# Optimization experiments

Hardware: AMD Instinct MI355X
Metric: run time of the kernel (lower is better)

Reference implementation:

```python
import jax, jax.numpy as jnp
import numpy as np

WINDOW = 7
EPS = 1e-8


def setup_inputs() -> dict:
    key = jax.random.key(0)
    k1, k2, k3 = jax.random.split(key, 3)
    x = jax.random.normal(k1, (8, 256, 64, 64), dtype=jnp.float32)
    # 1x1 conv weights (bias=False): [out_ch, in_ch]
    w_reduce = jax.random.normal(k2, (64, 256), dtype=jnp.float32) * 0.05
    w_proj = jax.random.normal(k3, (512, 64), dtype=jnp.float32) * 0.1
    return {"x": x, "w_reduce": w_reduce, "w_proj": w_proj}


def _unfold_window(feat, window):
    # feat: [b, c, h, w] -> patches: [b, c, window*window, h, w]
    b, c, h, w = feat.shape
    pad = window // 2
    fp = jnp.pad(feat, ((0, 0), (0, 0), (pad, pad), (pad, pad)))
    # fixed small loop over window^2 = 49 shifts (matches F.unfold ordering)
    return jnp.stack(
        [fp[:, :, i:i + h, j:j + w] for i in range(window) for j in range(window)],
        axis=2,
    )


def reference(x, w_reduce, w_proj):
    window = WINDOW
    # reduce: 1x1 conv, no bias
    feat = jnp.einsum('oc,bchw->bohw', w_reduce, x)  # [b, cr, h, w]
    patches = _unfold_window(feat, window)           # [b, cr, K, h, w], K=49
    # cosine similarity between center feature and each window patch (dim=channel)
    dot = jnp.einsum('bchw,bckhw->bkhw', feat, patches)          # [b, K, h, w]
    cn = jnp.sqrt(jnp.sum(feat * feat, axis=1))                  # [b, h, w]
    pn = jnp.sqrt(jnp.sum(patches * patches, axis=1))            # [b, K, h, w]
    sim = dot / jnp.maximum(cn[:, None] * pn, EPS)               # [b, K, h, w]
    att = jax.nn.softmax(sim, axis=1)                            # softmax over window dim
    corr = jnp.einsum('bkhw,bckhw->bchw', att, patches)          # [b, cr, h, w]
    # proj: 1x1 conv, no bias
    return jnp.einsum('oc,bchw->bohw', w_proj, corr)             # [b, out, h, w]
```

## Files before the change

kernel.cpp:

```cpp
#include <hip/hip_runtime.h>
#include <stdint.h>

#define NPIX 4096
#define CIN  256
#define CR   64
#define COUT 512
#define NB   8
#define CG   256
#define FT   128

typedef _Float16 half8 __attribute__((ext_vector_type(8)));
typedef float f32x4 __attribute__((ext_vector_type(4)));

__device__ __forceinline__ float dpp8_sum(float d) {
  int y;
  y = __builtin_amdgcn_update_dpp(0, __float_as_int(d), 0xB1, 0xF, 0xF, true);
  d += __int_as_float(y);
  y = __builtin_amdgcn_update_dpp(0, __float_as_int(d), 0x4E, 0xF, 0xF, true);
  d += __int_as_float(y);
  y = __builtin_amdgcn_update_dpp(0, __float_as_int(d), 0x141, 0xF, 0xF, true);
  d += __int_as_float(y);
  return d;
}

__global__ __launch_bounds__(256) void k0_prep(
    const float* __restrict__ wr, const float* __restrict__ wp,
    _Float16* __restrict__ wrAh, _Float16* __restrict__ wrAl,
    _Float16* __restrict__ wpH,
    float* __restrict__ cnormG, float* __restrict__ featTail)
{
  const int tid = blockIdx.x * 256 + threadIdx.x;
  if (tid < 16384) {
    const int j = tid & 7, l = (tid >> 3) & 63;
    const int kt = (tid >> 9) & 7, mt = tid >> 12;
    const int m = mt * 16 + (l & 15);
    const int k = kt * 32 + (l >> 4) * 8 + j;
    const float v = wr[m * CIN + k];
    const _Float16 h = (_Float16)v;
    wrAh[tid] = h;
    wrAl[tid] = (_Float16)(v - (float)h);
  } else if (tid < 16384 + COUT * CR) {
    const int fi = tid - 16384;
    const int j = fi & 7, l = (fi >> 3) & 63;
    const int kt = (fi >> 9) & 1, ot = (fi >> 10) & 3, g = fi >> 12;
    const int o = g * 64 + ot * 16 + (l & 15);
    const int k = kt * 32 + (l >> 4) * 8 + j;
    wpH[fi] = (_Float16)wp[o * CR + k];
  } else {
    const int gi = tid - (16384 + COUT * CR);
    if (gi < CG)               cnormG[gi] = 0.f;
    else if (gi < 2 * CG)      cnormG[CG + NB * NPIX + (gi - CG)] = 0.f;
    else if (gi < 2 * CG + FT) featTail[gi - 2 * CG] = 0.f;
  }
}

__global__ __launch_bounds__(512) void k1_reduce(
    const float* __restrict__ x,
    const _Float16* __restrict__ wrAh, const _Float16* __restrict__ wrAl,
    float* __restrict__ feat, float* __restrict__ cnorm)
{
  const int blk = blockIdx.x;
  const int b = blk >> 6, seg = blk & 63;
  const int t = threadIdx.x, lane = t & 63;
  const int g = __builtin_amdgcn_readfirstlane((int)t >> 6);
  const int nt = g & 3, mth = g >> 2;
  const int col = lane & 15, krow = lane >> 4;

  const float* xb = x + (size_t)b * CIN * NPIX + seg * 64 + nt * 16 + col;

  f32x4 c0 = {0.f, 0.f, 0.f, 0.f};
  f32x4 c1 = {0.f, 0.f, 0.f, 0.f};

#pragma unroll
  for (int kt = 0; kt < 8; ++kt) {
    half8 Bh, Bl;
    const float* xk = xb + (size_t)(kt * 32 + krow * 8) * NPIX;
#pragma unroll
    for (int j = 0; j < 8; ++j) {
      const float v = xk[(size_t)j * NPIX];
      const _Float16 h = (_Float16)v;
      Bh[j] = h;
      Bl[j] = (_Float16)(v - (float)h);
    }
    const int fi0 = ((mth * 2 + 0) * 8 + kt) * 512 + lane * 8;
    const int fi1 = ((mth * 2 + 1) * 8 + kt) * 512 + lane * 8;
    const half8 Ah0 = *(const half8*)(wrAh + fi0);
    const half8 Al0 = *(const half8*)(wrAl + fi0);
    const half8 Ah1 = *(const half8*)(wrAh + fi1);
    const half8 Al1 = *(const half8*)(wrAl + fi1);
    c0 = __builtin_amdgcn_mfma_f32_16x16x32_f16(Ah0, Bh, c0, 0, 0, 0);
    c0 = __builtin_amdgcn_mfma_f32_16x16x32_f16(Ah0, Bl, c0, 0, 0, 0);
    c0 = __builtin_amdgcn_mfma_f32_16x16x32_f16(Al0, Bh, c0, 0, 0, 0);
    c1 = __builtin_amdgcn_mfma_f32_16x16x32_f16(Ah1, Bh, c1, 0, 0, 0);
    c1 = __builtin_amdgcn_mfma_f32_16x16x32_f16(Ah1, Bl, c1, 0, 0, 0);
    c1 = __builtin_amdgcn_mfma_f32_16x16x32_f16(Al1, Bh, c1, 0, 0, 0);
  }

  float p = 0.f;
  float* fbase = feat + (size_t)b * CR * NPIX + seg * 64 + nt * 16 + col;
#pragma unroll
  for (int r = 0; r < 4; ++r) {
    const int m0 = (mth * 2 + 0) * 16 + krow * 4 + r;
    const int m1 = (mth * 2 + 1) * 16 + krow * 4 + r;
    fbase[(size_t)m0 * NPIX] = c0[r];
    fbase[(size_t)m1 * NPIX] = c1[r];
    p = fmaf(c0[r], c0[r], p);
    p = fmaf(c1[r], c1[r], p);
  }
  p += __shfl_xor(p, 16);
  p += __shfl_xor(p, 32);

  __shared__ float cn[8][16];
  if (lane < 16) cn[g][lane] = p;
  __syncthreads();
  if (t < 64) {
    const int nt2 = t >> 4, c16 = t & 15;
    cnorm[b * NPIX + seg * 64 + t] = sqrtf(cn[nt2][c16] + cn[nt2 + 4][c16]);
  }
}

__global__ __launch_bounds__(512, 4) void k23_fused(
    const float* __restrict__ feat, const float* __restrict__ cnorm,
    const _Float16* __restrict__ wpH, float* __restrict__ out)
{
  const int blk = blockIdx.x;
  const int b = blk & 7, h = blk >> 3;
  const int t = threadIdx.x;
  const int lane = t & 63;
  const int g = __builtin_amdgcn_readfirstlane((int)t >> 6);
  const int w = t >> 3;
  const int cb = (t & 7) * 8;
  const int px = h * 64 + w;
  const int gpx = b * NPIX + px;

  const float* fb = feat + (size_t)b * CR * NPIX;
  const float* cnb = cnorm + b * NPIX;

  __shared__ float fs[2][72][68];
  __shared__ float cnS[2][80];
  __shared__ __align__(16) _Float16 corrH[4096];

  float rA[2][4];
  float rB[4];
  float rc = 0.f;
  const int jt = 64 + (t >> 4), c4t = t & 15;

  auto LOAD = [&](int ar) {
    const int base = ar * 64 - 4;
#pragma unroll
    for (int k = 0; k < 2; ++k) {
      const int c4 = g * 2 + k;
#pragma unroll
      for (int q = 0; q < 4; ++q)
        rA[k][q] = fb[(size_t)(c4 * 4 + q) * NPIX + base + lane];
    }
    if (t < 128) {
#pragma unroll
      for (int q = 0; q < 4; ++q)
        rB[q] = fb[(size_t)(c4t * 4 + q) * NPIX + base + jt];
    }
    if (t < 72) rc = cnb[base + t];
  };
  auto WRITE = [&](int bufi) {
#pragma unroll
    for (int k = 0; k < 2; ++k) {
      const int c4 = g * 2 + k;
      *(float4*)&fs[bufi][lane][c4 * 4] =
          make_float4(rA[k][0], rA[k][1], rA[k][2], rA[k][3]);
    }
    if (t < 128)
      *(float4*)&fs[bufi][jt][c4t * 4] = make_float4(rB[0], rB[1], rB[2], rB[3]);
    if (t < 72) cnS[bufi][t] = rc;
  };

  const float* fpx = fb + (size_t)cb * NPIX + px;
  float fc[8];
#pragma unroll
  for (int i = 0; i < 8; ++i) fc[i] = fpx[i * NPIX];
  const float cnc = cnorm[gpx];

  float acc[8];
#pragma unroll
  for (int i = 0; i < 8; ++i) acc[i] = 0.f;

  const int lo = (h - 3 < 0) ? 0 : h - 3;
  const int hi = (h + 3 > 63) ? 63 : h + 3;
  float l = 7.0f * (float)(6 - (hi - lo));

  LOAD(lo);
  WRITE(0);
  __syncthreads();

  int buf = 0;
  for (int ar = lo; ar <= hi; ++ar) {
    if (ar < hi) LOAD(ar + 1);
#pragma unroll
    for (int dx = -3; dx <= 3; ++dx) {
      const int j = w + 4 + dx;
      const float4 nv0 = *(const float4*)&fs[buf][j][cb];
      const float4 nv1 = *(const float4*)&fs[buf][j][cb + 4];
      float d = fmaf(fc[0], nv0.x,
                fmaf(fc[1], nv0.y,
                fmaf(fc[2], nv0.z,
                fmaf(fc[3], nv0.w,
                fmaf(fc[4], nv1.x,
                fmaf(fc[5], nv1.y,
                fmaf(fc[6], nv1.z, fc[7] * nv1.w)))))));
      d = dpp8_sum(d);
      const float cnk = cnS[buf][j];
      float sim = d * __builtin_amdgcn_rcpf(fmaxf(cnc * cnk, 1e-8f));
      const bool valid = (unsigned)(w + dx) < 64u;
      sim = valid ? sim : 0.f;
      const float p = __expf(sim);
      l += p;
      const float pv = valid ? p : 0.f;
      acc[0] = fmaf(pv, nv0.x, acc[0]);
      acc[1] = fmaf(pv, nv0.y, acc[1]);
      acc[2] = fmaf(pv, nv0.z, acc[2]);
      acc[3] = fmaf(pv, nv0.w, acc[3]);
      acc[4] = fmaf(pv, nv1.x, acc[4]);
      acc[5] = fmaf(pv, nv1.y, acc[5]);
      acc[6] = fmaf(pv, nv1.z, acc[6]);
      acc[7] = fmaf(pv, nv1.w, acc[7]);
    }
    if (ar < hi) WRITE(buf ^ 1);
    __syncthreads();
    buf ^= 1;
  }

  {
    const float inv = __builtin_amdgcn_rcpf(l);
    half8 hv;
#pragma unroll
    for (int i = 0; i < 8; ++i) hv[i] = (_Float16)(acc[i] * inv);
    const int wbyte = (w * 128 + (cb << 1)) ^ ((w & 7) << 4);
    *(half8*)((char*)corrH + wbyte) = hv;
  }
  __syncthreads();

  const _Float16* wA = wpH + (size_t)g * 4096;
  float* outb = out + ((size_t)b * COUT + g * 64) * NPIX + h * 64;
#pragma unroll
  for (int pt = 0; pt < 4; ++pt) {
    half8 Bf0, Bf1;
    {
      const int pxl = pt * 16 + (lane & 15);
      const int sw = (pxl & 7) << 4;
      const int rowb = pxl * 128 + ((lane >> 4) << 4);
      Bf0 = *(const half8*)((const char*)corrH + (rowb ^ sw));
      Bf1 = *(const half8*)((const char*)corrH + ((rowb + 64) ^ sw));
    }
#pragma unroll
    for (int ot = 0; ot < 4; ++ot) {
      f32x4 c = {0.f, 0.f, 0.f, 0.f};
      const half8 A0 = *(const half8*)(wA + (ot * 2 + 0) * 512 + lane * 8);
      const half8 A1 = *(const half8*)(wA + (ot * 2 + 1) * 512 + lane * 8);
      c = __builtin_amdgcn_mfma_f32_16x16x32_f16(A0, Bf0, c, 0, 0, 0);
      c = __builtin_amdgcn_mfma_f32_16x16x32_f16(A1, Bf1, c, 0, 0, 0);
      float* op = outb + (size_t)(ot * 16 + ((lane >> 4) << 2)) * NPIX
                       + pt * 16 + (lane & 15);
#pragma unroll
      for (int r = 0; r < 4; ++r) op[(size_t)r * NPIX] = c[r];
    }
  }
}

extern "C" void kernel_launch(void* const* d_in, const int* in_sizes, int n_in,
                              void* d_out, int out_size, void* d_ws, size_t ws_size,
                              hipStream_t stream)
{
  const float* x  = (const float*)d_in[0];
  const float* wr = (const float*)d_in[1];
  const float* wp = (const float*)d_in[2];
  float* out = (float*)d_out;

  float* ws = (float*)d_ws;
  _Float16* wrAh  = (_Float16*)ws;
  _Float16* wrAl  = (_Float16*)(ws + 8192);
  _Float16* wpH   = (_Float16*)(ws + 16384);
  float* cnormG   = ws + 32768;
  float* cnorm    = cnormG + CG;
  float* feat     = cnorm + NB * NPIX + CG;
  float* featTail = feat + (size_t)NB * CR * NPIX;

  hipLaunchKernelGGL(k0_prep,   dim3(195), dim3(256), 0, stream, wr, wp, wrAh, wrAl, wpH, cnormG, featTail);
  hipLaunchKernelGGL(k1_reduce, dim3(512), dim3(512), 0, stream, x, wrAh, wrAl, feat, cnorm);
  hipLaunchKernelGGL(k23_fused, dim3(512), dim3(512), 0, stream, feat, cnorm, wpH, out);
}
```

Measured before the change: 46.19 us.

## Store reduced features as fp16 pixel-major and use packed half math

The intermediate feature tensor is now stored as fp16 in a pixel-major [b][pixel][channel] layout instead of fp32 channel-major. This halves its global traffic and makes row loads into shared memory contiguous. The window loop uses fdot2 for the dot products and packed half2 FMAs for the weighted accumulation, split across two accumulator sets. The cost is lower precision in both the cosine similarities and the accumulated correlation sums, which may exceed the output tolerance. cnorm is still computed in fp32.

Result: faster. 41.10 us (-11.0%).

```diff
diff --git a/kernel.cpp b/kernel.cpp
--- a/kernel.cpp
+++ b/kernel.cpp
@@ -10,6 +10,8 @@
 #define FT   128
 
 typedef _Float16 half8 __attribute__((ext_vector_type(8)));
+typedef _Float16 half4 __attribute__((ext_vector_type(4)));
+typedef _Float16 half2v __attribute__((ext_vector_type(2)));
 typedef float f32x4 __attribute__((ext_vector_type(4)));
 
 __device__ __forceinline__ float dpp8_sum(float d) {
@@ -57,7 +59,7 @@
 __global__ __launch_bounds__(512) void k1_reduce(
     const float* __restrict__ x,
     const _Float16* __restrict__ wrAh, const _Float16* __restrict__ wrAl,
-    float* __restrict__ feat, float* __restrict__ cnorm)
+    _Float16* __restrict__ feat_h, float* __restrict__ cnorm)
 {
   const int blk = blockIdx.x;
   const int b = blk >> 6, seg = blk & 63;
@@ -96,17 +98,21 @@
     c1 = __builtin_amdgcn_mfma_f32_16x16x32_f16(Al1, Bh, c1, 0, 0, 0);
   }
 
+  const int px = seg * 64 + nt * 16 + col;
+  _Float16* fb = feat_h + ((size_t)b * NPIX + px) * 64;
+  const int ch0 = mth * 32 + krow * 4;
+  half4 v0, v1;
   float p = 0.f;
-  float* fbase = feat + (size_t)b * CR * NPIX + seg * 64 + nt * 16 + col;
 #pragma unroll
   for (int r = 0; r < 4; ++r) {
-    const int m0 = (mth * 2 + 0) * 16 + krow * 4 + r;
-    const int m1 = (mth * 2 + 1) * 16 + krow * 4 + r;
-    fbase[(size_t)m0 * NPIX] = c0[r];
-    fbase[(size_t)m1 * NPIX] = c1[r];
+    v0[r] = (_Float16)c0[r];
+    v1[r] = (_Float16)c1[r];
     p = fmaf(c0[r], c0[r], p);
     p = fmaf(c1[r], c1[r], p);
   }
+  *(half4*)(fb + ch0) = v0;
+  *(half4*)(fb + ch0 + 16) = v1;
+
   p += __shfl_xor(p, 16);
   p += __shfl_xor(p, 32);
 
@@ -120,7 +126,7 @@
 }
 
 __global__ __launch_bounds__(512, 4) void k23_fused(
-    const float* __restrict__ feat, const float* __restrict__ cnorm,
+    const _Float16* __restrict__ feat_h, const float* __restrict__ cnorm,
     const _Float16* __restrict__ wpH, float* __restrict__ out)
 {
   const int blk = blockIdx.x;
@@ -133,55 +139,41 @@
   const int px = h * 64 + w;
   const int gpx = b * NPIX + px;
 
-  const float* fb = feat + (size_t)b * CR * NPIX;
   const float* cnb = cnorm + b * NPIX;
 
-  __shared__ float fs[2][72][68];
+  __shared__ __align__(16) _Float16 fs[2][72][72];
   __shared__ float cnS[2][80];
   __shared__ __align__(16) _Float16 corrH[4096];
 
-  float rA[2][4];
-  float rB[4];
+  half8 rS0, rS1;
   float rc = 0.f;
-  const int jt = 64 + (t >> 4), c4t = t & 15;
 
   auto LOAD = [&](int ar) {
-    const int base = ar * 64 - 4;
-#pragma unroll
-    for (int k = 0; k < 2; ++k) {
-      const int c4 = g * 2 + k;
-#pragma unroll
-      for (int q = 0; q < 4; ++q)
-        rA[k][q] = fb[(size_t)(c4 * 4 + q) * NPIX + base + lane];
-    }
-    if (t < 128) {
-#pragma unroll
-      for (int q = 0; q < 4; ++q)
-        rB[q] = fb[(size_t)(c4t * 4 + q) * NPIX + base + jt];
-    }
-    if (t < 72) rc = cnb[base + t];
+    const long rowb = ((long)b * NPIX + ar * 64 - 4) * 64;
+    rS0 = *(const half8*)(feat_h + rowb + (long)t * 8);
+    if (t < 64) rS1 = *(const half8*)(feat_h + rowb + (long)(512 + t) * 8);
+    if (t < 72) rc = cnb[ar * 64 - 4 + t];
   };
   auto WRITE = [&](int bufi) {
-#pragma unroll
-    for (int k = 0; k < 2; ++k) {
-      const int c4 = g * 2 + k;
-      *(float4*)&fs[bufi][lane][c4 * 4] =
-          make_float4(rA[k][0], rA[k][1], rA[k][2], rA[k][3]);
-    }
-    if (t < 128)
-      *(float4*)&fs[bufi][jt][c4t * 4] = make_float4(rB[0], rB[1], rB[2], rB[3]);
+    *(half8*)&fs[bufi][t >> 3][(t & 7) * 8] = rS0;
+    if (t < 64) *(half8*)&fs[bufi][64 + (t >> 3)][(t & 7) * 8] = rS1;
     if (t < 72) cnS[bufi][t] = rc;
   };
 
-  const float* fpx = fb + (size_t)cb * NPIX + px;
-  float fc[8];
-#pragma unroll
-  for (int i = 0; i < 8; ++i) fc[i] = fpx[i * NPIX];
+  half2v fc2[4];
+  {
+    const half8 fcv = *(const half8*)(feat_h + ((size_t)b * NPIX + px) * 64 + cb);
+#pragma unroll
+    for (int i = 0; i < 4; ++i) { fc2[i][0] = fcv[2*i]; fc2[i][1] = fcv[2*i+1]; }
+  }
   const float cnc = cnorm[gpx];
 
-  float acc[8];
-#pragma unroll
-  for (int i = 0; i < 8; ++i) acc[i] = 0.f;
+  half2v accA[4], accB[4];
+#pragma unroll
+  for (int i = 0; i < 4; ++i) {
+    accA[i] = (half2v)(_Float16)0.f;
+    accB[i] = (half2v)(_Float16)0.f;
+  }
 
   const int lo = (h - 3 < 0) ? 0 : h - 3;
   const int hi = (h + 3 > 63) ? 63 : h + 3;
@@ -197,15 +189,17 @@
 #pragma unroll
     for (int dx = -3; dx <= 3; ++dx) {
       const int j = w + 4 + dx;
-      const float4 nv0 = *(const float4*)&fs[buf][j][cb];
-      const float4 nv1 = *(const float4*)&fs[buf][j][cb + 4];
-      float d = fmaf(fc[0], nv0.x,
-                fmaf(fc[1], nv0.y,
-                fmaf(fc[2], nv0.z,
-                fmaf(fc[3], nv0.w,
-                fmaf(fc[4], nv1.x,
-                fmaf(fc[5], nv1.y,
-                fmaf(fc[6], nv1.z, fc[7] * nv1.w)))))));
+      const half8 nv = *(const half8*)&fs[buf][j][cb];
+      half2v n0, n1, n2, n3;
+      n0[0] = nv[0]; n0[1] = nv[1];
+      n1[0] = nv[2]; n1[1] = nv[3];
+      n2[0] = nv[4]; n2[1] = nv[5];
+      n3[0] = nv[6]; n3[1] = nv[7];
+      float d = 0.f;
+      d = __builtin_amdgcn_fdot2(fc2[0], n0, d, false);
+      d = __builtin_amdgcn_fdot2(fc2[1], n1, d, false);
+      d = __builtin_amdgcn_fdot2(fc2[2], n2, d, false);
+      d = __builtin_amdgcn_fdot2(fc2[3], n3, d, false);
       d = dpp8_sum(d);
       const float cnk = cnS[buf][j];
       float sim = d * __builtin_amdgcn_rcpf(fmaxf(cnc * cnk, 1e-8f));
@@ -214,14 +208,19 @@
       const float p = __expf(sim);
       l += p;
       const float pv = valid ? p : 0.f;
-      acc[0] = fmaf(pv, nv0.x, acc[0]);
-      acc[1] = fmaf(pv, nv0.y, acc[1]);
-      acc[2] = fmaf(pv, nv0.z, acc[2]);
-      acc[3] = fmaf(pv, nv0.w, acc[3]);
-      acc[4] = fmaf(pv, nv1.x, acc[4]);
-      acc[5] = fmaf(pv, nv1.y, acc[5]);
-      acc[6] = fmaf(pv, nv1.z, acc[6]);
-      acc[7] = fmaf(pv, nv1.w, acc[7]);
+      const _Float16 ph = (_Float16)pv;
+      half2v ph2; ph2[0] = ph; ph2[1] = ph;
+      if (dx & 1) {
+        accA[0] = ph2 * n0 + accA[0];
+        accA[1] = ph2 * n1 + accA[1];
+        accA[2] = ph2 * n2 + accA[2];
+        accA[3] = ph2 * n3 + accA[3];
+      } else {
+        accB[0] = ph2 * n0 + accB[0];
+        accB[1] = ph2 * n1 + accB[1];
+        accB[2] = ph2 * n2 + accB[2];
+        accB[3] = ph2 * n3 + accB[3];
+      }
     }
     if (ar < hi) WRITE(buf ^ 1);
     __syncthreads();
@@ -232,7 +231,12 @@
     const float inv = __builtin_amdgcn_rcpf(l);
     half8 hv;
 #pragma unroll
-    for (int i = 0; i < 8; ++i) hv[i] = (_Float16)(acc[i] * inv);
+    for (int i = 0; i < 4; ++i) {
+      const float a0 = (float)accA[i][0] + (float)accB[i][0];
+      const float a1 = (float)accA[i][1] + (float)accB[i][1];
+      hv[2*i]   = (_Float16)(a0 * inv);
+      hv[2*i+1] = (_Float16)(a1 * inv);
+    }
     const int wbyte = (w * 128 + (cb << 1)) ^ ((w & 7) << 4);
     *(half8*)((char*)corrH + wbyte) = hv;
   }
@@ -280,10 +284,10 @@
   _Float16* wpH   = (_Float16*)(ws + 16384);
   float* cnormG   = ws + 32768;
   float* cnorm    = cnormG + CG;
-  float* feat     = cnorm + NB * NPIX + CG;
-  float* featTail = feat + (size_t)NB * CR * NPIX;
+  _Float16* feat_h = (_Float16*)(cnorm + NB * NPIX + CG);
+  float* featTail = (float*)(feat_h + (size_t)NB * NPIX * 64);
 
   hipLaunchKernelGGL(k0_prep,   dim3(195), dim3(256), 0, stream, wr, wp, wrAh, wrAl, wpH, cnormG, featTail);
-  hipLaunchKernelGGL(k1_reduce, dim3(512), dim3(512), 0, stream, x, wrAh, wrAl, feat, cnorm);
-  hipLaunchKernelGGL(k23_fused, dim3(512), dim3(512), 0, stream, feat, cnorm, wpH, out);
-}
+  hipLaunchKernelGGL(k1_reduce, dim3(512), dim3(512), 0, stream, x, wrAh, wrAl, feat_h, cnorm);
+  hipLaunchKernelGGL(k23_fused, dim3(512), dim3(512), 0, stream, feat_h, cnorm, wpH, out);
+}
```
